# Optimization experiments

Hardware: AMD Instinct MI355X
Metric: run time of the kernel (lower is better)

The kernel has to match this reference:

```python
import jax, jax.numpy as jnp
import numpy as np

B, C, H, W = 16, 256, 32, 32
N_HEAD, DIM_HEAD = 8, 32  # dim_hidden = 256 == C


def setup_inputs() -> dict:
    key = jax.random.key(0)
    ks = jax.random.split(key, 9)
    s = 1.0 / np.sqrt(C)
    return {
        "x": jax.random.normal(ks[0], (B, C, H, W), dtype=jnp.float32),
        "w_q": jax.random.normal(ks[1], (C, C), dtype=jnp.float32) * s,
        "b_q": jnp.zeros((C,), dtype=jnp.float32),
        "w_k": jax.random.normal(ks[2], (C, C), dtype=jnp.float32) * s,
        "b_k": jnp.zeros((C,), dtype=jnp.float32),
        "w_v": jax.random.normal(ks[3], (C, C), dtype=jnp.float32) * s,
        "b_v": jnp.zeros((C,), dtype=jnp.float32),
        "w_o": jax.random.normal(ks[4], (C, C), dtype=jnp.float32) * s,
        "b_o": jnp.zeros((C,), dtype=jnp.float32),
    }


def reference(x, w_q, b_q, w_k, b_k, w_v, b_v, w_o, b_o):
    b, c, h, w = x.shape
    L = h * w
    scale = DIM_HEAD ** (-0.5)
    xf = x.reshape(b, c, L)  # [b, c, L]

    def proj(wm, bm):
        # 1x1 conv == per-position linear over channels
        y = jnp.einsum('oc,bcl->bol', wm, xf) + bm[None, :, None]
        return y.reshape(b, N_HEAD, DIM_HEAD, L)

    q = proj(w_q, b_q) * scale
    k = proj(w_k, b_k)
    v = proj(w_v, b_v)

    sim = jnp.einsum('bndl,bndm->bnlm', q, k)           # [b, n, L, L]
    att = jax.nn.softmax(sim, axis=-1)
    out = jnp.einsum('bnlm,bndm->bndl', att, v)         # [b, n, d, L]
    out = out.reshape(b, c, L)
    out = jnp.einsum('oc,bcl->bol', w_o, out) + b_o[None, :, None]
    return out.reshape(b, c, h, w)
```

## Files before the change

### kernel.cpp

```cpp
#include <hip/hip_runtime.h>
#include <hip/hip_bf16.h>
#include <math.h>

namespace {
constexpr int B_ = 16, C_ = 256, L_ = 1024, NH_ = 8, DH_ = 32;

typedef __attribute__((ext_vector_type(8))) short short8v;
typedef __attribute__((ext_vector_type(4))) float float4v;

__device__ __forceinline__ short f2bf(float f) {
    unsigned u = __builtin_bit_cast(unsigned, f);
    u += 0x7fffu + ((u >> 16) & 1u);
    return (short)(u >> 16);
}
__device__ __forceinline__ float bf2f(short s) {
    unsigned u = ((unsigned)(unsigned short)s) << 16;
    return __builtin_bit_cast(float, u);
}
__device__ __forceinline__ unsigned pkrn(float a, float b) {
    float2 f; f.x = a; f.y = b;
    __hip_bfloat162 h = __float22bfloat162_rn(f);
    unsigned u;
    __builtin_memcpy(&u, &h, sizeof(u));
    return u;
}
__device__ __forceinline__ void gld16(const short* g, short* l) {
    __builtin_amdgcn_global_load_lds(
        (const __attribute__((address_space(1))) unsigned*)g,
        (__attribute__((address_space(3))) unsigned*)l, 16, 0, 0);
}

__global__ __launch_bounds__(256) void prep_kernel(
    const float* __restrict__ x, short* __restrict__ xthi,
    const float* __restrict__ wq, const float* __restrict__ wk,
    const float* __restrict__ wv, const float* __restrict__ wo,
    short* __restrict__ WA, short* __restrict__ WoA)
{
    const int bid = blockIdx.x;
    const int t = threadIdx.x;
    __shared__ float sX[64][68];

    if (bid < 1024) {
        const int lt = bid & 15, ct = (bid >> 4) & 3, b = bid >> 6;
#pragma unroll
        for (int e = 0; e < 4; ++e) {
            const int row = e * 16 + (t >> 4);
            const int col = (t & 15) * 4;
            float4 v = *(const float4*)&x[((size_t)b * C_ + ct * 64 + row) * L_ + lt * 64 + col];
            *(float4*)&sX[row][col] = v;
        }
        __syncthreads();

        const int l = t & 63, cg = t >> 6;
        short hi[16];
#pragma unroll
        for (int i = 0; i < 16; ++i) hi[i] = f2bf(sX[cg * 16 + i][l]);
        const size_t base = ((size_t)b * L_ + lt * 64 + l) * C_ + ct * 64 + cg * 16;
        *(short8v*)&xthi[base]     = *(short8v*)&hi[0];
        *(short8v*)&xthi[base + 8] = *(short8v*)&hi[8];
    } else {
        const int g = (bid - 1024) * 256 + t;
        if (g < 768 * 256) {
            const int o = g >> 8, cc = g & 255;
            const float* src = (o < 256) ? wq : (o < 512) ? wk : wv;
            WA[(size_t)o * 256 + cc] = f2bf(src[(size_t)(o & 255) * 256 + cc]);
        } else {
            const int g2 = g - 768 * 256;
            const int o = g2 >> 8, cc = g2 & 255;
            WoA[(size_t)o * 256 + cc] = f2bf(wo[(size_t)o * 256 + cc]);
        }
    }
}

template <int KTOT, int EPI>
__global__ __launch_bounds__(256, 4) void gemm_kernel(
    const short* __restrict__ A, const short* __restrict__ B0,
    const float* __restrict__ bias0, const float* __restrict__ bias1, const float* __restrict__ bias2,
    float qscale, void* __restrict__ out0, void* __restrict__ out1, void* __restrict__ out2)
{
    const int lt = blockIdx.x, ot = blockIdx.y, b = blockIdx.z;
    const int t = threadIdx.x, wv = t >> 6, lane = t & 63;
    const int quad = lane >> 4, c = lane & 15;
    const int wo = (wv & 1) * 64;
    const int wl = (wv >> 1) * 32;

    __shared__ short sA[128 * 64];
    __shared__ short sB[64 * 64];

    float4v acc[4][2];
#pragma unroll
    for (int i = 0; i < 4; ++i)
#pragma unroll
        for (int j = 0; j < 2; ++j) acc[i][j] = (float4v)0.f;

    const short* Arow = A + (size_t)(ot * 128) * KTOT;
    const int srow = t >> 3, sseg = t & 7;
    const int seg = sseg ^ (srow & 7);

    for (int kk = 0; kk < KTOT / 64; ++kk) {
        __syncthreads();
#pragma unroll
        for (int e = 0; e < 4; ++e)
            gld16(Arow + (size_t)(e * 32 + srow) * KTOT + kk * 64 + seg * 8,
                  &sA[(e * 256 + t) * 8]);
#pragma unroll
        for (int e = 0; e < 2; ++e)
            gld16(B0 + ((size_t)b * L_ + lt * 64 + e * 32 + srow) * 256 + kk * 64 + seg * 8,
                  &sB[(e * 256 + t) * 8]);
        __syncthreads();

#pragma unroll
        for (int kc2 = 0; kc2 < 2; ++kc2) {
            short8v af[4], bf[2];
#pragma unroll
            for (int i = 0; i < 4; ++i) {
                const int row = wo + 16 * i + c;
                af[i] = *(const short8v*)&sA[row * 64 + (((kc2 * 4 + quad) ^ (c & 7)) * 8)];
            }
#pragma unroll
            for (int j = 0; j < 2; ++j) {
                const int row = wl + 16 * j + c;
                bf[j] = *(const short8v*)&sB[row * 64 + (((kc2 * 4 + quad) ^ (c & 7)) * 8)];
            }
#pragma unroll
            for (int i = 0; i < 4; ++i)
#pragma unroll
                for (int j = 0; j < 2; ++j)
                    acc[i][j] = __builtin_amdgcn_mfma_f32_16x16x32_bf16(af[i], bf[j], acc[i][j], 0, 0, 0);
        }
    }

    if constexpr (EPI == 0) {
        const int typ = ot >> 1;
        const int chbase = (ot & 1) * 128 + wo;
        const float* bp = (typ == 0) ? bias0 : (typ == 1) ? bias1 : bias2;
        const float sc = (typ == 0) ? qscale : 1.f;
        short* outp = (short*)((typ == 0) ? out0 : (typ == 1) ? out1 : out2);
        if (typ < 2) {
#pragma unroll
            for (int i = 0; i < 4; ++i) {
                const int ch0 = chbase + 16 * i + quad * 4;
                const int head = ch0 >> 5, d0 = ch0 & 31;
                float bias[4];
#pragma unroll
                for (int r = 0; r < 4; ++r) bias[r] = bp[ch0 + r];
#pragma unroll
                for (int j = 0; j < 2; ++j) {
                    const int l = lt * 64 + wl + 16 * j + c;
                    short4 sv;
                    sv.x = f2bf((acc[i][j][0] + bias[0]) * sc);
                    sv.y = f2bf((acc[i][j][1] + bias[1]) * sc);
                    sv.z = f2bf((acc[i][j][2] + bias[2]) * sc);
                    sv.w = f2bf((acc[i][j][3] + bias[3]) * sc);
                    *(short4*)&outp[(((size_t)b * NH_ + head) * L_ + l) * 32 + d0] = sv;
                }
            }
        } else {
#pragma unroll
            for (int i = 0; i < 4; ++i)
#pragma unroll
                for (int r = 0; r < 4; ++r) {
                    const int ch = chbase + 16 * i + quad * 4 + r;
                    const float bias = bp[ch];
#pragma unroll
                    for (int j = 0; j < 2; ++j)
                        outp[((size_t)b * C_ + ch) * L_ + lt * 64 + wl + 16 * j + c] =
                            f2bf(acc[i][j][r] + bias);
                }
        }
    } else {
        float* outp = (float*)out0;
#pragma unroll
        for (int i = 0; i < 4; ++i)
#pragma unroll
            for (int r = 0; r < 4; ++r) {
                const int ch = ot * 128 + wo + 16 * i + quad * 4 + r;
                const float bias = bias0[ch];
#pragma unroll
                for (int j = 0; j < 2; ++j)
                    outp[((size_t)b * C_ + ch) * L_ + lt * 64 + wl + 16 * j + c] =
                        acc[i][j][r] + bias;
            }
    }
}

__global__ __launch_bounds__(256, 4) void attn_kernel(
    const short* __restrict__ qt,
    const short* __restrict__ kt,
    const short* __restrict__ vb,
    short* __restrict__ athi)
{
    const int flat = blockIdx.x;
    const int g = ((flat >> 6) << 3) | (flat & 7);
    const int chunk = (flat >> 3) & 7;
    const int b = g >> 3, h = g & 7;
    const int t = threadIdx.x;
    const int wv = t >> 6, lane = t & 63;
    const int quad = lane >> 4, c = lane & 15;
    const int lq0 = chunk * 128 + wv * 32;

    __shared__ __align__(16) short sK[2][64 * 32];
    __shared__ __align__(16) short sV[2][2][32 * 32];
    __shared__ __align__(16) short sPT[4][2][16][64];

    const size_t bh = (size_t)b * NH_ + h;
    const short* qbase = qt + (bh * L_) * 32;
    const short* kbase = kt + (bh * L_) * 32;
    const size_t vrow = (size_t)b * C_ + h * DH_;

    short8v qfrag[2];
#pragma unroll
    for (int qf = 0; qf < 2; ++qf)
        qfrag[qf] = *(const short8v*)(qbase + (size_t)(lq0 + qf * 16 + c) * 32 + quad * 8);

    float lp4[2][4];
#pragma unroll
    for (int qf = 0; qf < 2; ++qf)
#pragma unroll
        for (int r = 0; r < 4; ++r) lp4[qf][r] = 0.f;
    float4v o_acc[2][2];
#pragma unroll
    for (int qf = 0; qf < 2; ++qf) { o_acc[qf][0] = (float4v)0.f; o_acc[qf][1] = (float4v)0.f; }

    const int sseg = (t & 3) ^ ((t >> 3) & 3);
    const int rsw = (c >> 1) & 3;

    auto stage = [&](int m0, int buf) {
        gld16(kbase + (size_t)(m0 + (t >> 2)) * 32 + sseg * 8, &sK[buf][t * 8]);
        gld16(vb + (vrow + ((t >> 2) & 31)) * L_ + m0 + (t >> 7) * 32 + sseg * 8,
              (short*)sV[buf] + t * 8);
    };

    stage(0, 0);

    short8v vfp[2][2];

    for (int i = 0; i <= 16; ++i) {
        short8v kf[4], vf[2][2];
        if (i < 16) {
            __syncthreads();
            if (i < 15) stage((i + 1) * 64, (i + 1) & 1);
            const short* Kb = sK[i & 1];
            const short* Vb = (const short*)sV[i & 1];
#pragma unroll
            for (int kb = 0; kb < 4; ++kb)
                kf[kb] = *(const short8v*)&Kb[(kb * 16 + c) * 32 + ((quad ^ rsw) * 8)];
#pragma unroll
            for (int kc = 0; kc < 2; ++kc)
#pragma unroll
                for (int nb2 = 0; nb2 < 2; ++nb2)
                    vf[kc][nb2] = *(const short8v*)&Vb[kc * 1024 + (nb2 * 16 + c) * 32 + ((quad ^ rsw) * 8)];
        }

        if (i > 0) {
#pragma unroll
            for (int qf = 0; qf < 2; ++qf)
#pragma unroll
                for (int kc = 0; kc < 2; ++kc) {
                    const int G = (kc * 4 + quad) ^ (c & 7);
                    const short8v pf = *(const short8v*)&sPT[wv][qf][c][G * 8];
#pragma unroll
                    for (int nb2 = 0; nb2 < 2; ++nb2)
                        o_acc[qf][nb2] = __builtin_amdgcn_mfma_f32_16x16x32_bf16(vfp[kc][nb2], pf, o_acc[qf][nb2], 0, 0, 0);
                }
        }

        if (i < 16) {
            float4v st[2][4];
#pragma unroll
            for (int qf = 0; qf < 2; ++qf)
#pragma unroll
                for (int kb = 0; kb < 4; ++kb)
                    st[qf][kb] = __builtin_amdgcn_mfma_f32_16x16x32_bf16(kf[kb], qfrag[qf], (float4v)0.f, 0, 0, 0);
#pragma unroll
            for (int qf = 0; qf < 2; ++qf)
#pragma unroll
                for (int kb = 0; kb < 4; ++kb) {
                    float p[4];
#pragma unroll
                    for (int r = 0; r < 4; ++r) {
                        p[r] = __builtin_amdgcn_exp2f(st[qf][kb][r]);
                        lp4[qf][r] += p[r];
                    }
                    uint2 w;
                    w.x = pkrn(p[0], p[1]);
                    w.y = pkrn(p[2], p[3]);
                    const int Gw = (kb * 2 + (quad >> 1)) ^ (c & 7);
                    *(uint2*)&sPT[wv][qf][c][Gw * 8 + (quad & 1) * 4] = w;
                }
#pragma unroll
            for (int kc = 0; kc < 2; ++kc)
#pragma unroll
                for (int nb2 = 0; nb2 < 2; ++nb2) vfp[kc][nb2] = vf[kc][nb2];
        }
    }

#pragma unroll
    for (int qf = 0; qf < 2; ++qf) {
        float l = (lp4[qf][0] + lp4[qf][1]) + (lp4[qf][2] + lp4[qf][3]);
        l += __shfl_xor(l, 16);
        l += __shfl_xor(l, 32);
        const float inv = 1.f / l;
#pragma unroll
        for (int nb2 = 0; nb2 < 2; ++nb2) {
            short4 sv;
            sv.x = f2bf(o_acc[qf][nb2][0] * inv);
            sv.y = f2bf(o_acc[qf][nb2][1] * inv);
            sv.z = f2bf(o_acc[qf][nb2][2] * inv);
            sv.w = f2bf(o_acc[qf][nb2][3] * inv);
            *(short4*)&athi[((size_t)b * L_ + lq0 + qf * 16 + c) * C_ + h * DH_ + nb2 * 16 + quad * 4] = sv;
        }
    }
}

}

extern "C" void kernel_launch(void* const* d_in, const int* in_sizes, int n_in,
                              void* d_out, int out_size, void* d_ws, size_t ws_size,
                              hipStream_t stream) {
    const float* x   = (const float*)d_in[0];
    const float* w_q = (const float*)d_in[1];
    const float* b_q = (const float*)d_in[2];
    const float* w_k = (const float*)d_in[3];
    const float* b_k = (const float*)d_in[4];
    const float* w_v = (const float*)d_in[5];
    const float* b_v = (const float*)d_in[6];
    const float* w_o = (const float*)d_in[7];
    const float* b_o = (const float*)d_in[8];
    float* out = (float*)d_out;

    const size_t NT = (size_t)B_ * L_ * C_;
    short* xthi = (short*)d_ws;
    short* WA   = xthi + NT;
    short* WoA  = WA + 768 * 256;
    short* qt   = WoA + 256 * 256;
    short* kt   = qt + NT;
    short* vb   = kt + NT;
    short* athi = vb + NT;

    const float scale_q = 0.17677669529663687f * 1.4426950408889634f;

    prep_kernel<<<dim3(2048), 256, 0, stream>>>(x, xthi, w_q, w_k, w_v, w_o, WA, WoA);
    gemm_kernel<256, 0><<<dim3(L_ / 64, 6, B_), 256, 0, stream>>>(
        WA, xthi, b_q, b_k, b_v, scale_q, qt, kt, vb);
    attn_kernel<<<dim3(1024), 256, 0, stream>>>(qt, kt, vb, athi);
    gemm_kernel<256, 1><<<dim3(L_ / 64, 2, B_), 256, 0, stream>>>(
        WoA, athi, b_o, nullptr, nullptr, 1.f, out, nullptr, nullptr);
}
```

Before: 140.1 us.

## Fuse x transpose and bf16 conversion into QKV GEMM B-tile load

Removes the separate transpose/convert pass over x by having the QKV GEMM read fp32 x directly, convert to bf16 and write the swizzled B tile into LDS. The weight-conversion kernel is also vectorized with float4 loads and short4 stores. This avoids a full write and re-read of the bf16 transposed activation buffer. In exchange, the GEMM's B loads become synchronous register loads instead of async global-to-LDS copies, and the 6 output-tile blocks per position each re-read and re-convert x.

```diff
diff --git a/kernel.cpp b/kernel.cpp
--- a/kernel.cpp
+++ b/kernel.cpp
@@ -12,10 +12,6 @@
     unsigned u = __builtin_bit_cast(unsigned, f);
     u += 0x7fffu + ((u >> 16) & 1u);
     return (short)(u >> 16);
-}
-__device__ __forceinline__ float bf2f(short s) {
-    unsigned u = ((unsigned)(unsigned short)s) << 16;
-    return __builtin_bit_cast(float, u);
 }
 __device__ __forceinline__ unsigned pkrn(float a, float b) {
     float2 f; f.x = a; f.y = b;
@@ -30,51 +26,26 @@
         (__attribute__((address_space(3))) unsigned*)l, 16, 0, 0);
 }
 
-__global__ __launch_bounds__(256) void prep_kernel(
-    const float* __restrict__ x, short* __restrict__ xthi,
+__global__ __launch_bounds__(256) void prepw_kernel(
     const float* __restrict__ wq, const float* __restrict__ wk,
     const float* __restrict__ wv, const float* __restrict__ wo,
     short* __restrict__ WA, short* __restrict__ WoA)
 {
-    const int bid = blockIdx.x;
-    const int t = threadIdx.x;
-    __shared__ float sX[64][68];
-
-    if (bid < 1024) {
-        const int lt = bid & 15, ct = (bid >> 4) & 3, b = bid >> 6;
-#pragma unroll
-        for (int e = 0; e < 4; ++e) {
-            const int row = e * 16 + (t >> 4);
-            const int col = (t & 15) * 4;
-            float4 v = *(const float4*)&x[((size_t)b * C_ + ct * 64 + row) * L_ + lt * 64 + col];
-            *(float4*)&sX[row][col] = v;
-        }
-        __syncthreads();
-
-        const int l = t & 63, cg = t >> 6;
-        short hi[16];
-#pragma unroll
-        for (int i = 0; i < 16; ++i) hi[i] = f2bf(sX[cg * 16 + i][l]);
-        const size_t base = ((size_t)b * L_ + lt * 64 + l) * C_ + ct * 64 + cg * 16;
-        *(short8v*)&xthi[base]     = *(short8v*)&hi[0];
-        *(short8v*)&xthi[base + 8] = *(short8v*)&hi[8];
-    } else {
-        const int g = (bid - 1024) * 256 + t;
-        if (g < 768 * 256) {
-            const int o = g >> 8, cc = g & 255;
-            const float* src = (o < 256) ? wq : (o < 512) ? wk : wv;
-            WA[(size_t)o * 256 + cc] = f2bf(src[(size_t)(o & 255) * 256 + cc]);
-        } else {
-            const int g2 = g - 768 * 256;
-            const int o = g2 >> 8, cc = g2 & 255;
-            WoA[(size_t)o * 256 + cc] = f2bf(wo[(size_t)o * 256 + cc]);
-        }
-    }
-}
-
-template <int KTOT, int EPI>
+    const int g4 = blockIdx.x * 256 + threadIdx.x;
+    const int o = g4 >> 6, cc = (g4 & 63) * 4;
+    const float* src = (o < 256) ? wq : (o < 512) ? wk : (o < 768) ? wv : wo;
+    const float4 v = *(const float4*)&src[(size_t)(o & 255) * 256 + cc];
+    short4 s;
+    s.x = f2bf(v.x); s.y = f2bf(v.y); s.z = f2bf(v.z); s.w = f2bf(v.w);
+    short* dst = (o < 768) ? &WA[(size_t)o * 256 + cc]
+                           : &WoA[(size_t)(o - 768) * 256 + cc];
+    *(short4*)dst = s;
+}
+
+template <int KTOT, int EPI, int TRANS>
 __global__ __launch_bounds__(256, 4) void gemm_kernel(
     const short* __restrict__ A, const short* __restrict__ B0,
+    const float* __restrict__ X,
     const float* __restrict__ bias0, const float* __restrict__ bias1, const float* __restrict__ bias2,
     float qscale, void* __restrict__ out0, void* __restrict__ out1, void* __restrict__ out2)
 {
@@ -103,10 +74,23 @@
         for (int e = 0; e < 4; ++e)
             gld16(Arow + (size_t)(e * 32 + srow) * KTOT + kk * 64 + seg * 8,
                   &sA[(e * 256 + t) * 8]);
-#pragma unroll
-        for (int e = 0; e < 2; ++e)
-            gld16(B0 + ((size_t)b * L_ + lt * 64 + e * 32 + srow) * 256 + kk * 64 + seg * 8,
-                  &sB[(e * 256 + t) * 8]);
+        if constexpr (TRANS) {
+            const int lrow = t & 63, w8 = t >> 6;
+            const float* xcol = X + ((size_t)b * C_ + kk * 64 + w8 * 16) * L_ + lt * 64 + lrow;
+            float vv[16];
+#pragma unroll
+            for (int j = 0; j < 16; ++j) vv[j] = xcol[(size_t)j * L_];
+            unsigned pk[8];
+#pragma unroll
+            for (int j = 0; j < 8; ++j) pk[j] = pkrn(vv[2 * j], vv[2 * j + 1]);
+            *(uint4*)&sB[(lrow * 8 + ((2 * w8)     ^ (lrow & 7))) * 8] = *(uint4*)&pk[0];
+            *(uint4*)&sB[(lrow * 8 + ((2 * w8 + 1) ^ (lrow & 7))) * 8] = *(uint4*)&pk[4];
+        } else {
+#pragma unroll
+            for (int e = 0; e < 2; ++e)
+                gld16(B0 + ((size_t)b * L_ + lt * 64 + e * 32 + srow) * 256 + kk * 64 + seg * 8,
+                      &sB[(e * 256 + t) * 8]);
+        }
         __syncthreads();
 
 #pragma unroll
@@ -330,8 +314,7 @@
     float* out = (float*)d_out;
 
     const size_t NT = (size_t)B_ * L_ * C_;
-    short* xthi = (short*)d_ws;
-    short* WA   = xthi + NT;
+    short* WA   = (short*)d_ws;
     short* WoA  = WA + 768 * 256;
     short* qt   = WoA + 256 * 256;
     short* kt   = qt + NT;
@@ -340,10 +323,10 @@
 
     const float scale_q = 0.17677669529663687f * 1.4426950408889634f;
 
-    prep_kernel<<<dim3(2048), 256, 0, stream>>>(x, xthi, w_q, w_k, w_v, w_o, WA, WoA);
-    gemm_kernel<256, 0><<<dim3(L_ / 64, 6, B_), 256, 0, stream>>>(
-        WA, xthi, b_q, b_k, b_v, scale_q, qt, kt, vb);
+    prepw_kernel<<<dim3(256), 256, 0, stream>>>(w_q, w_k, w_v, w_o, WA, WoA);
+    gemm_kernel<256, 0, 1><<<dim3(L_ / 64, 6, B_), 256, 0, stream>>>(
+        WA, nullptr, x, b_q, b_k, b_v, scale_q, qt, kt, vb);
     attn_kernel<<<dim3(1024), 256, 0, stream>>>(qt, kt, vb, athi);
-    gemm_kernel<256, 1><<<dim3(L_ / 64, 2, B_), 256, 0, stream>>>(
-        WoA, athi, b_o, nullptr, nullptr, 1.f, out, nullptr, nullptr);
-}
+    gemm_kernel<256, 1, 0><<<dim3(L_ / 64, 2, B_), 256, 0, stream>>>(
+        WoA, athi, nullptr, b_o, nullptr, nullptr, 1.f, out, nullptr, nullptr);
+}
```

Result: faster. 135.4 us (-3.3%).
